# Kernel tuning notes

Measured on AMD Instinct MI355X. Metric: run time of the kernel, lower is better.

Reference implementation:

```python
import jax, jax.numpy as jnp
import numpy as np

A, B, K, P, STRIDE = 32, 32, 3, 4, 2
C = P * P          # 16
D = P * P          # 16 (not last layer)
KK = K * K
KKA = KK * A       # 288
BN_EPS = 1e-5


def _unfold(x, k, s):
    """torch.nn.functional.unfold (pad=0): [b,c,h,w] -> [b, c*k*k, l],
    channel-major then kernel-position ordering (matches torch)."""
    b, c, h, w = x.shape
    oh = (h - k) // s + 1
    ow = (w - k) // s + 1
    patches = jnp.stack(
        [x[:, :, i:i + s * oh:s, j:j + s * ow:s] for i in range(k) for j in range(k)],
        axis=2,
    )  # [b, c, kk, oh, ow]
    return patches.reshape(b, c * k * k, oh * ow)


def setup_inputs() -> dict:
    key = jax.random.key(0)
    k1, k2, k3, k4, k5 = jax.random.split(key, 5)
    b, h, w = 16, 14, 14
    a = jax.random.uniform(k1, (b, A, h, w), dtype=jnp.float32)
    pose = jax.random.normal(k2, (b, A * C, h, w), dtype=jnp.float32)
    # kaiming_uniform over [kkA, B*D, C]: fan_in = C (last dim of matmul weight rows)
    bound1 = float(np.sqrt(6.0 / C))
    W1 = jax.random.uniform(k3, (KKA, B * D, C), minval=-bound1, maxval=bound1, dtype=jnp.float32)
    W2 = jax.random.normal(k4, (KKA, B, C), dtype=jnp.float32) * 0.1
    b2 = jax.random.normal(k5, (1, 1, KKA, B), dtype=jnp.float32) * 0.1
    bn_gamma = jnp.ones((B * D,), dtype=jnp.float32)
    bn_beta = jnp.zeros((B * D,), dtype=jnp.float32)
    return {"a": a, "pose": pose, "W1": W1, "W2": W2, "b2": b2,
            "bn_gamma": bn_gamma, "bn_beta": bn_beta}


def reference(a, pose, W1, W2, b2, bn_gamma, bn_beta):
    b, _, h, w = a.shape
    oh = (h - K) // STRIDE + 1
    ow = (w - K) // STRIDE + 1
    l = oh * ow

    # ---- pose patches: [b, l, kkA, C] (kk-major, A-minor) ----
    pose_u = _unfold(pose, K, STRIDE)                      # [b, A*C*kk, l]
    pose_u = pose_u.reshape(b, A, C, KK, l)
    pose_u = pose_u.transpose(0, 4, 3, 1, 2).reshape(b, l, KKA, C)

    # ---- per-patch small GEMVs ----
    pose_out = jnp.einsum('nmc,blnc->blnm', W1, pose_u)    # [b, l, kkA, B*D]
    pose_out = pose_out.reshape(b, l, KKA, B, D)
    logit = jnp.einsum('njc,blnc->blnj', W2, pose_u) + b2  # [b, l, kkA, B]
    r = jax.nn.softmax(logit, axis=3)

    # ---- activation patches: [b, l, kkA, 1] ----
    a_u = _unfold(a, K, STRIDE).reshape(b, A, KK, l)
    a_u = a_u.transpose(0, 3, 2, 1).reshape(b, l, KKA, 1)

    # ---- routing-weighted reduction ----
    ar = a_u * r                                           # [b, l, kkA, B]
    ar_sum = ar.sum(axis=2, keepdims=True)                 # [b, l, 1, B]
    coeff = (ar / ar_sum)[..., None]                       # [b, l, kkA, B, 1]
    a_out = (ar_sum / a_u.sum(axis=2, keepdims=True)).squeeze(2)  # [b, l, B]
    a_out = a_out.transpose(0, 2, 1).reshape(b, B, oh, ow)

    pose_o = (coeff * pose_out).sum(axis=2)                # [b, l, B, D]
    pose_o = pose_o.reshape(b, l, B * D).transpose(0, 2, 1).reshape(b, B * D, oh, ow)

    # ---- BatchNorm2d (training-mode batch stats, biased var, eps=1e-5) ----
    mean = pose_o.mean(axis=(0, 2, 3), keepdims=True)
    var = pose_o.var(axis=(0, 2, 3), keepdims=True)
    pose_o = (pose_o - mean) * jax.lax.rsqrt(var + BN_EPS)
    pose_o = pose_o * bn_gamma.reshape(1, -1, 1, 1) + bn_beta.reshape(1, -1, 1, 1)
    return a_out, pose_o
```

## Files before the change

### kernel.cpp

```cpp
#include <hip/hip_runtime.h>

#define AA 32
#define BB 32
#define CC 16
#define KKA 288
#define OHW 6
#define LL 36
#define NBL 576
#define HH 14
#define WWD 14

#define W1B_OFF   0ull
#define W2B_OFF   2359296ull
#define PU16_OFF  2506752ull
#define AR16_OFF  5160960ull
#define FREG_BYTE 20938752ull
#define AU_F      0ull
#define ARSUMP_F  165888ull
#define INV_F     497664ull
#define PREP_F    516096ull

typedef __attribute__((ext_vector_type(8))) short bf16x8;
typedef __attribute__((ext_vector_type(4))) float f32x4;
typedef __attribute__((ext_vector_type(16))) float f32x16;

__device__ __forceinline__ unsigned cvtpk(float lo, float hi) {
    unsigned r;
    asm("v_cvt_pk_bf16_f32 %0, %1, %2" : "=v"(r) : "v"(lo), "v"(hi));
    return r;
}
__device__ __forceinline__ float blo(unsigned u) {
    return __builtin_bit_cast(float, u << 16);
}
__device__ __forceinline__ float bhi(unsigned u) {
    return __builtin_bit_cast(float, u & 0xffff0000u);
}

__global__ __launch_bounds__(256) void k_prep(
    const float* __restrict__ W1, const float* __restrict__ W2,
    const float* __restrict__ a, const float* __restrict__ pose,
    unsigned short* __restrict__ W1b, unsigned short* __restrict__ W2b,
    unsigned short* __restrict__ pu16, float* __restrict__ auf)
{
    __shared__ float ps[16][196];
    __shared__ float as_[196];
    const int tid = threadIdx.x;

    if (blockIdx.x < 1224) {
        size_t i = ((size_t)blockIdx.x * 256 + tid) * 8;
        const float* src;
        unsigned short* dst;
        if (i < 2359296ull) { src = W1 + i; dst = W1b + i; }
        else { src = W2 + (i - 2359296ull); dst = W2b + (i - 2359296ull); }
        float4 v0 = *reinterpret_cast<const float4*>(src);
        float4 v1 = *reinterpret_cast<const float4*>(src + 4);
        uint4 o;
        o.x = cvtpk(v0.x, v0.y);
        o.y = cvtpk(v0.z, v0.w);
        o.z = cvtpk(v1.x, v1.y);
        o.w = cvtpk(v1.z, v1.w);
        *reinterpret_cast<uint4*>(dst) = o;
        return;
    }

    const int bid = blockIdx.x - 1224;
    const int b = bid >> 5, aidx = bid & 31;

    const float* psrc = pose + ((size_t)b * 512 + (size_t)aidx * 16) * 196;
    for (int t = tid; t < 3136; t += 256) ((float*)ps)[t] = psrc[t];
    const float* asrc = a + ((size_t)b * 32 + aidx) * 196;
    if (tid < 196) as_[tid] = asrc[tid];
    __syncthreads();

    for (int t = tid; t < 1296; t += 256) {
        int quad = t & 3;
        int l = (t >> 2) % 36;
        int kk = t / 144;
        int oy = l / 6, ox = l - (l / 6) * 6;
        int ki = kk / 3, kj = kk - (kk / 3) * 3;
        int pix = (oy * 2 + ki) * 14 + ox * 2 + kj;
        uint2 v;
        v.x = cvtpk(ps[quad * 4 + 0][pix], ps[quad * 4 + 1][pix]);
        v.y = cvtpk(ps[quad * 4 + 2][pix], ps[quad * 4 + 3][pix]);
        *reinterpret_cast<uint2*>(
            pu16 + (((size_t)(kk * 32 + aidx)) * 576 + b * 36 + l) * 16 + quad * 4) = v;
    }
    for (int t = tid; t < 324; t += 256) {
        int kk = t % 9, l = t / 9;
        int oy = l / 6, ox = l - (l / 6) * 6;
        int ki = kk / 3, kj = kk - (kk / 3) * 3;
        auf[((size_t)(b * 36 + l)) * KKA + kk * 32 + aidx] =
            as_[(oy * 2 + ki) * 14 + ox * 2 + kj];
    }
}

__global__ __launch_bounds__(256) void k_logit(
    const unsigned short* __restrict__ W2b, const unsigned short* __restrict__ pu16,
    const float* __restrict__ b2, const float* __restrict__ auf,
    unsigned* __restrict__ aru, float* __restrict__ arsump)
{
    __shared__ float b2_s[16][32];
    __shared__ float au_s[16][17];
    __shared__ float asum_s[4][16][32];
    const int bl0 = blockIdx.x * 16;
    const int n0b = blockIdx.y * 16;
    const int tid = threadIdx.x;

    #pragma unroll
    for (int k = 0; k < 2; ++k) {
        int t = tid + k * 256;
        b2_s[t >> 5][t & 31] = b2[(size_t)(n0b + (t >> 5)) * 32 + (t & 31)];
    }
    {
        int blr = tid >> 4, nl = tid & 15;
        au_s[blr][nl] = auf[((size_t)(bl0 + blr)) * KKA + n0b + nl];
    }
    __syncthreads();

    const int w = tid >> 6, lane = tid & 63;
    const int g = lane >> 4, d = lane & 15;
    float asum[8] = {0.f, 0.f, 0.f, 0.f, 0.f, 0.f, 0.f, 0.f};

    #pragma unroll
    for (int nn = 0; nn < 4; ++nn) {
        const int nl = w * 4 + nn;
        const int n  = n0b + nl;
        uint4 a0 = {0, 0, 0, 0}, a1 = {0, 0, 0, 0}, bbv = {0, 0, 0, 0};
        if (g < 2) {
            a0 = *reinterpret_cast<const uint4*>(W2b + ((size_t)n * 32 + d) * 16 + g * 8);
            a1 = *reinterpret_cast<const uint4*>(W2b + ((size_t)n * 32 + 16 + d) * 16 + g * 8);
            bbv = *reinterpret_cast<const uint4*>(
                pu16 + ((size_t)n * 576 + bl0 + d) * 16 + g * 8);
        }
        f32x4 zero = {0.f, 0.f, 0.f, 0.f};
        f32x4 c0 = __builtin_amdgcn_mfma_f32_16x16x32_bf16(
            __builtin_bit_cast(bf16x8, a0), __builtin_bit_cast(bf16x8, bbv), zero, 0, 0, 0);
        f32x4 c1 = __builtin_amdgcn_mfma_f32_16x16x32_bf16(
            __builtin_bit_cast(bf16x8, a1), __builtin_bit_cast(bf16x8, bbv), zero, 0, 0, 0);

        float v[8];
        float s = 0.f;
        #pragma unroll
        for (int i = 0; i < 4; ++i) {
            v[i]     = __expf(c0[i] + b2_s[nl][g * 4 + i]);
            v[4 + i] = __expf(c1[i] + b2_s[nl][16 + g * 4 + i]);
            s += v[i] + v[4 + i];
        }
        s += __shfl_xor(s, 16);
        s += __shfl_xor(s, 32);
        const float scale = au_s[d][nl] / s;
        float p[8];
        #pragma unroll
        for (int i = 0; i < 8; ++i) { p[i] = v[i] * scale; asum[i] += p[i]; }

        aru[((size_t)n * 16 + g * 2    ) * 576 + bl0 + d] = cvtpk(p[0], p[1]);
        aru[((size_t)n * 16 + g * 2 + 1) * 576 + bl0 + d] = cvtpk(p[2], p[3]);
        aru[((size_t)n * 16 + 8 + g * 2    ) * 576 + bl0 + d] = cvtpk(p[4], p[5]);
        aru[((size_t)n * 16 + 8 + g * 2 + 1) * 576 + bl0 + d] = cvtpk(p[6], p[7]);
    }
    #pragma unroll
    for (int i = 0; i < 4; ++i) {
        asum_s[w][d][g * 4 + i]      = asum[i];
        asum_s[w][d][16 + g * 4 + i] = asum[4 + i];
    }
    __syncthreads();
    #pragma unroll
    for (int k = 0; k < 2; ++k) {
        int idx = tid + k * 256;
        int dd = idx >> 5, j = idx & 31;
        float s = asum_s[0][dd][j] + asum_s[1][dd][j] + asum_s[2][dd][j] + asum_s[3][dd][j];
        arsump[(size_t)blockIdx.y * 18432 + ((size_t)(bl0 + dd)) * 32 + j] = s;
    }
}

__global__ __launch_bounds__(256) void k_finish(
    const float* __restrict__ arsump, const float* __restrict__ auf,
    float* __restrict__ invarsum, float* __restrict__ out_a)
{
    const int tid = threadIdx.x;
    const int wid = tid >> 6, lane = tid & 63;
    const int bl = blockIdx.x * 4 + wid;
    const int j = lane & 31, h = lane >> 5;

    float s = 0.f;
    #pragma unroll
    for (int k = 0; k < 9; ++k) {
        int r = h * 9 + k;
        s += arsump[(size_t)r * 18432 + (size_t)bl * 32 + j];
    }
    s += __shfl_xor(s, 32);

    float at = 0.f;
    #pragma unroll
    for (int k = 0; k < 5; ++k) {
        int n = k * 64 + lane;
        if (n < KKA) at += auf[(size_t)bl * KKA + n];
    }
    #pragma unroll
    for (int m = 1; m <= 32; m <<= 1) at += __shfl_xor(at, m);

    if (lane < 32) {
        invarsum[(size_t)j * 576 + bl] = 1.0f / s;
        int b = bl / 36, l = bl - (bl / 36) * 36;
        out_a[((size_t)b * 32 + j) * 36 + l] = s / at;
    }
}

__global__ __launch_bounds__(256) void k_pose(
    const unsigned short* __restrict__ W1b, const unsigned short* __restrict__ pu16,
    const unsigned* __restrict__ aru, const float* __restrict__ invarsum,
    float* __restrict__ prep)
{
    __shared__ float red_s[3][16][64];

    const int bid = blockIdx.x;
    const int wg  = (bid & 7) * 144 + (bid >> 3);
    const int q   = wg / 288;
    const int rem = wg - q * 288;
    const int jp  = rem / 18;
    const int bl0 = (rem - jp * 18) * 32;

    const int tid = threadIdx.x;
    const int w = tid >> 6, lane = tid & 63;
    const int col = lane & 31, kg = lane >> 5;

    const unsigned short* wp = W1b + ((size_t)(jp * 32 + col)) * 16 + kg * 8;
    const unsigned short* pp = pu16 + ((size_t)(bl0 + col)) * 16 + kg * 8;
    const unsigned* ap = aru + (size_t)jp * 576 + bl0 + col;
    const int n0 = q * 72 + w * 18;

    float acc[16];
    #pragma unroll
    for (int i = 0; i < 16; ++i) acc[i] = 0.f;
    f32x16 zv = {0.f,0.f,0.f,0.f,0.f,0.f,0.f,0.f,0.f,0.f,0.f,0.f,0.f,0.f,0.f,0.f};

    #pragma unroll 6
    for (int i = 0; i < 18; ++i) {
        const size_t n = (size_t)(n0 + i);
        uint4 a4 = *reinterpret_cast<const uint4*>(wp + n * 8192);
        uint4 b4 = *reinterpret_cast<const uint4*>(pp + n * 9216);
        unsigned av = ap[n * 9216];
        f32x16 cd = __builtin_amdgcn_mfma_f32_32x32x16_bf16(
            __builtin_bit_cast(bf16x8, a4), __builtin_bit_cast(bf16x8, b4),
            zv, 0, 0, 0);
        float slo = blo(av), shi = bhi(av);
        #pragma unroll
        for (int r = 0; r < 8; ++r)  acc[r] = fmaf(cd[r], slo, acc[r]);
        #pragma unroll
        for (int r = 8; r < 16; ++r) acc[r] = fmaf(cd[r], shi, acc[r]);
    }

    if (w > 0) {
        #pragma unroll
        for (int i = 0; i < 16; ++i) red_s[w - 1][i][lane] = acc[i];
    }
    __syncthreads();
    if (w == 0) {
        const float ilo = invarsum[(size_t)(jp * 2) * 576 + bl0 + col];
        const float ihi = invarsum[(size_t)(jp * 2 + 1) * 576 + bl0 + col];
        #pragma unroll
        for (int i = 0; i < 16; ++i) {
            float v = acc[i] + red_s[0][i][lane] + red_s[1][i][lane] + red_s[2][i][lane];
            int r = (i & 3) + 8 * (i >> 2) + 4 * kg;
            float vv = v * (i < 8 ? ilo : ihi);
            prep[((size_t)q * 512 + jp * 32 + r) * NBL + bl0 + col] = vv;
        }
    }
}

__global__ __launch_bounds__(256) void k_bn(
    const float* __restrict__ prep, const float* __restrict__ gamma,
    const float* __restrict__ beta, float* __restrict__ out_pose)
{
    const int tid = threadIdx.x;
    const int wid = tid >> 6, lane = tid & 63;
    const int ch  = blockIdx.x * 4 + wid;
    const float* p0 = prep + (size_t)ch * NBL;

    float sum = 0.f, sq = 0.f;
    float v[9];
    #pragma unroll
    for (int k = 0; k < 9; ++k) {
        int i = lane + k * 64;
        float x = p0[i] + p0[i + 294912] + p0[i + 2 * 294912] + p0[i + 3 * 294912];
        v[k] = x;
        sum += x;
        sq  += x * x;
    }
    #pragma unroll
    for (int msk = 32; msk >= 1; msk >>= 1) {
        sum += __shfl_xor(sum, msk);
        sq  += __shfl_xor(sq, msk);
    }
    const float mean = sum * (1.f / 576.f);
    const float var  = sq * (1.f / 576.f) - mean * mean;
    const float inv  = rsqrtf(var + 1e-5f);
    const float sc   = gamma[ch] * inv;
    const float sh   = beta[ch] - mean * sc;
    #pragma unroll
    for (int k = 0; k < 9; ++k) {
        int i = lane + k * 64;
        int b = i / 36;
        int l = i - b * 36;
        out_pose[(size_t)b * 18432 + (size_t)ch * 36 + l] = v[k] * sc + sh;
    }
}

extern "C" void kernel_launch(void* const* d_in, const int* in_sizes, int n_in,
                              void* d_out, int out_size, void* d_ws, size_t ws_size,
                              hipStream_t stream)
{
    const float* a     = (const float*)d_in[0];
    const float* pose  = (const float*)d_in[1];
    const float* W1    = (const float*)d_in[2];
    const float* W2    = (const float*)d_in[3];
    const float* b2    = (const float*)d_in[4];
    const float* gamma = (const float*)d_in[5];
    const float* beta  = (const float*)d_in[6];
    float* out      = (float*)d_out;
    float* out_a    = out;
    float* out_pose = out + 18432;

    unsigned short* wsu = (unsigned short*)d_ws;
    unsigned short* W1b   = wsu + W1B_OFF;
    unsigned short* W2b   = wsu + W2B_OFF;
    unsigned short* pu16  = wsu + PU16_OFF;
    unsigned*       aru   = (unsigned*)(wsu + AR16_OFF);
    float* wsf    = (float*)((char*)d_ws + FREG_BYTE);
    float* auf    = wsf + AU_F;
    float* arsump = wsf + ARSUMP_F;
    float* invv   = wsf + INV_F;
    float* prep   = wsf + PREP_F;

    hipLaunchKernelGGL(k_prep, dim3(1736), dim3(256), 0, stream,
                       W1, W2, a, pose, W1b, W2b, pu16, auf);
    hipLaunchKernelGGL(k_logit, dim3(36, 18), dim3(256), 0, stream,
                       W2b, pu16, b2, auf, aru, arsump);
    hipLaunchKernelGGL(k_finish, dim3(144), dim3(256), 0, stream,
                       arsump, auf, invv, out_a);
    hipLaunchKernelGGL(k_pose, dim3(1152), dim3(256), 0, stream,
                       W1b, pu16, aru, invv, prep);
    hipLaunchKernelGGL(k_bn, dim3(128), dim3(256), 0, stream,
                       prep, gamma, beta, out_pose);
}
```

Baseline: 38.99 us.

## Remove k_finish kernel by folding arsum reduction into k_pose and k_bn

The logit kernel moves from 16x16x32 MFMA tiles to a single 32x32x16 MFMA per n and writes its partial ar sums in a j-major [r][j][bl] layout. The separate k_finish launch is removed. k_pose now reduces the 36 partial sums itself to form the inverse ar_sum, and k_bn gains 16 extra blocks that compute a_out. This saves one kernel launch and its dependency barrier, but repeats the partial-sum reduction in every k_pose workgroup.

```diff
diff --git a/kernel.cpp b/kernel.cpp
--- a/kernel.cpp
+++ b/kernel.cpp
@@ -17,8 +17,7 @@
 #define FREG_BYTE 20938752ull
 #define AU_F      0ull
 #define ARSUMP_F  165888ull
-#define INV_F     497664ull
-#define PREP_F    516096ull
+#define PREP_F    829440ull
 
 typedef __attribute__((ext_vector_type(8))) short bf16x8;
 typedef __attribute__((ext_vector_type(4))) float f32x4;
@@ -99,116 +98,82 @@
     const float* __restrict__ b2, const float* __restrict__ auf,
     unsigned* __restrict__ aru, float* __restrict__ arsump)
 {
-    __shared__ float b2_s[16][32];
-    __shared__ float au_s[16][17];
-    __shared__ float asum_s[4][16][32];
-    const int bl0 = blockIdx.x * 16;
-    const int n0b = blockIdx.y * 16;
+    __shared__ float b2_s[8][32];
+    __shared__ float au_s[8][32];
+    __shared__ float asum_s[4][64][16];
+
+    const int bl0 = blockIdx.x * 32;
+    const int n0  = blockIdx.y * 8;
     const int tid = threadIdx.x;
-
-    #pragma unroll
-    for (int k = 0; k < 2; ++k) {
-        int t = tid + k * 256;
-        b2_s[t >> 5][t & 31] = b2[(size_t)(n0b + (t >> 5)) * 32 + (t & 31)];
-    }
+    const int w = tid >> 6, lane = tid & 63;
+    const int col = lane & 31, kg = lane >> 5;
+
     {
-        int blr = tid >> 4, nl = tid & 15;
-        au_s[blr][nl] = auf[((size_t)(bl0 + blr)) * KKA + n0b + nl];
-    }
-    __syncthreads();
-
-    const int w = tid >> 6, lane = tid & 63;
-    const int g = lane >> 4, d = lane & 15;
-    float asum[8] = {0.f, 0.f, 0.f, 0.f, 0.f, 0.f, 0.f, 0.f};
-
-    #pragma unroll
-    for (int nn = 0; nn < 4; ++nn) {
-        const int nl = w * 4 + nn;
-        const int n  = n0b + nl;
-        uint4 a0 = {0, 0, 0, 0}, a1 = {0, 0, 0, 0}, bbv = {0, 0, 0, 0};
-        if (g < 2) {
-            a0 = *reinterpret_cast<const uint4*>(W2b + ((size_t)n * 32 + d) * 16 + g * 8);
-            a1 = *reinterpret_cast<const uint4*>(W2b + ((size_t)n * 32 + 16 + d) * 16 + g * 8);
-            bbv = *reinterpret_cast<const uint4*>(
-                pu16 + ((size_t)n * 576 + bl0 + d) * 16 + g * 8);
-        }
-        f32x4 zero = {0.f, 0.f, 0.f, 0.f};
-        f32x4 c0 = __builtin_amdgcn_mfma_f32_16x16x32_bf16(
-            __builtin_bit_cast(bf16x8, a0), __builtin_bit_cast(bf16x8, bbv), zero, 0, 0, 0);
-        f32x4 c1 = __builtin_amdgcn_mfma_f32_16x16x32_bf16(
-            __builtin_bit_cast(bf16x8, a1), __builtin_bit_cast(bf16x8, bbv), zero, 0, 0, 0);
-
-        float v[8];
+        int nl = tid >> 5, j = tid & 31;
+        b2_s[nl][j] = b2[(size_t)(n0 + nl) * 32 + j];
+        int nl2 = tid & 7, blr = tid >> 3;
+        au_s[nl2][blr] = auf[((size_t)(bl0 + blr)) * KKA + n0 + nl2];
+    }
+    __syncthreads();
+
+    float asum[16];
+    #pragma unroll
+    for (int i = 0; i < 16; ++i) asum[i] = 0.f;
+    const f32x16 zv = {0.f,0.f,0.f,0.f,0.f,0.f,0.f,0.f,
+                       0.f,0.f,0.f,0.f,0.f,0.f,0.f,0.f};
+
+    #pragma unroll
+    for (int nn = 0; nn < 2; ++nn) {
+        const int nl = w * 2 + nn;
+        const int n  = n0 + nl;
+        uint4 a4 = *reinterpret_cast<const uint4*>(
+            W2b + ((size_t)n * 32 + col) * 16 + kg * 8);
+        uint4 b4 = *reinterpret_cast<const uint4*>(
+            pu16 + ((size_t)n * 576 + bl0 + col) * 16 + kg * 8);
+        f32x16 cd = __builtin_amdgcn_mfma_f32_32x32x16_bf16(
+            __builtin_bit_cast(bf16x8, a4), __builtin_bit_cast(bf16x8, b4),
+            zv, 0, 0, 0);
+
+        float p[16];
         float s = 0.f;
         #pragma unroll
-        for (int i = 0; i < 4; ++i) {
-            v[i]     = __expf(c0[i] + b2_s[nl][g * 4 + i]);
-            v[4 + i] = __expf(c1[i] + b2_s[nl][16 + g * 4 + i]);
-            s += v[i] + v[4 + i];
-        }
-        s += __shfl_xor(s, 16);
+        for (int m = 0; m < 4; ++m) {
+            float4 bb = *reinterpret_cast<const float4*>(&b2_s[nl][m * 8 + kg * 4]);
+            p[m * 4 + 0] = __expf(cd[m * 4 + 0] + bb.x);
+            p[m * 4 + 1] = __expf(cd[m * 4 + 1] + bb.y);
+            p[m * 4 + 2] = __expf(cd[m * 4 + 2] + bb.z);
+            p[m * 4 + 3] = __expf(cd[m * 4 + 3] + bb.w);
+            s += p[m*4+0] + p[m*4+1] + p[m*4+2] + p[m*4+3];
+        }
         s += __shfl_xor(s, 32);
-        const float scale = au_s[d][nl] / s;
-        float p[8];
-        #pragma unroll
-        for (int i = 0; i < 8; ++i) { p[i] = v[i] * scale; asum[i] += p[i]; }
-
-        aru[((size_t)n * 16 + g * 2    ) * 576 + bl0 + d] = cvtpk(p[0], p[1]);
-        aru[((size_t)n * 16 + g * 2 + 1) * 576 + bl0 + d] = cvtpk(p[2], p[3]);
-        aru[((size_t)n * 16 + 8 + g * 2    ) * 576 + bl0 + d] = cvtpk(p[4], p[5]);
-        aru[((size_t)n * 16 + 8 + g * 2 + 1) * 576 + bl0 + d] = cvtpk(p[6], p[7]);
-    }
-    #pragma unroll
-    for (int i = 0; i < 4; ++i) {
-        asum_s[w][d][g * 4 + i]      = asum[i];
-        asum_s[w][d][16 + g * 4 + i] = asum[4 + i];
-    }
-    __syncthreads();
-    #pragma unroll
-    for (int k = 0; k < 2; ++k) {
+        const float scale = au_s[nl][col] / s;
+        #pragma unroll
+        for (int i = 0; i < 16; ++i) { p[i] *= scale; asum[i] += p[i]; }
+
+        #pragma unroll
+        for (int t = 0; t < 8; ++t) {
+            int jp = (t & 1) + 4 * (t >> 1) + 2 * kg;
+            aru[((size_t)n * 16 + jp) * 576 + bl0 + col] =
+                cvtpk(p[2 * t], p[2 * t + 1]);
+        }
+    }
+    #pragma unroll
+    for (int i = 0; i < 16; ++i) asum_s[w][lane][i] = asum[i];
+    __syncthreads();
+    #pragma unroll
+    for (int k = 0; k < 4; ++k) {
         int idx = tid + k * 256;
-        int dd = idx >> 5, j = idx & 31;
-        float s = asum_s[0][dd][j] + asum_s[1][dd][j] + asum_s[2][dd][j] + asum_s[3][dd][j];
-        arsump[(size_t)blockIdx.y * 18432 + ((size_t)(bl0 + dd)) * 32 + j] = s;
-    }
-}
-
-__global__ __launch_bounds__(256) void k_finish(
-    const float* __restrict__ arsump, const float* __restrict__ auf,
-    float* __restrict__ invarsum, float* __restrict__ out_a)
-{
-    const int tid = threadIdx.x;
-    const int wid = tid >> 6, lane = tid & 63;
-    const int bl = blockIdx.x * 4 + wid;
-    const int j = lane & 31, h = lane >> 5;
-
-    float s = 0.f;
-    #pragma unroll
-    for (int k = 0; k < 9; ++k) {
-        int r = h * 9 + k;
-        s += arsump[(size_t)r * 18432 + (size_t)bl * 32 + j];
-    }
-    s += __shfl_xor(s, 32);
-
-    float at = 0.f;
-    #pragma unroll
-    for (int k = 0; k < 5; ++k) {
-        int n = k * 64 + lane;
-        if (n < KKA) at += auf[(size_t)bl * KKA + n];
-    }
-    #pragma unroll
-    for (int m = 1; m <= 32; m <<= 1) at += __shfl_xor(at, m);
-
-    if (lane < 32) {
-        invarsum[(size_t)j * 576 + bl] = 1.0f / s;
-        int b = bl / 36, l = bl - (bl / 36) * 36;
-        out_a[((size_t)b * 32 + j) * 36 + l] = s / at;
+        int L = idx & 63, i = idx >> 6;
+        float s = asum_s[0][L][i] + asum_s[1][L][i]
+                + asum_s[2][L][i] + asum_s[3][L][i];
+        int row = (i & 3) + 8 * (i >> 2) + 4 * (L >> 5);
+        arsump[((size_t)blockIdx.y * 32 + row) * 576 + bl0 + (L & 31)] = s;
     }
 }
 
 __global__ __launch_bounds__(256) void k_pose(
     const unsigned short* __restrict__ W1b, const unsigned short* __restrict__ pu16,
-    const unsigned* __restrict__ aru, const float* __restrict__ invarsum,
+    const unsigned* __restrict__ aru, const float* __restrict__ arsump,
     float* __restrict__ prep)
 {
     __shared__ float red_s[3][16][64];
@@ -223,6 +188,17 @@
     const int tid = threadIdx.x;
     const int w = tid >> 6, lane = tid & 63;
     const int col = lane & 31, kg = lane >> 5;
+
+    float ilo = 0.f, ihi = 0.f;
+    if (w == 0) {
+        #pragma unroll 9
+        for (int r = 0; r < 36; ++r) {
+            ilo += arsump[((size_t)r * 32 + jp * 2    ) * 576 + bl0 + col];
+            ihi += arsump[((size_t)r * 32 + jp * 2 + 1) * 576 + bl0 + col];
+        }
+        ilo = 1.0f / ilo;
+        ihi = 1.0f / ihi;
+    }
 
     const unsigned short* wp = W1b + ((size_t)(jp * 32 + col)) * 16 + kg * 8;
     const unsigned short* pp = pu16 + ((size_t)(bl0 + col)) * 16 + kg * 8;
@@ -256,8 +232,6 @@
     }
     __syncthreads();
     if (w == 0) {
-        const float ilo = invarsum[(size_t)(jp * 2) * 576 + bl0 + col];
-        const float ihi = invarsum[(size_t)(jp * 2 + 1) * 576 + bl0 + col];
         #pragma unroll
         for (int i = 0; i < 16; ++i) {
             float v = acc[i] + red_s[0][i][lane] + red_s[1][i][lane] + red_s[2][i][lane];
@@ -270,39 +244,66 @@
 
 __global__ __launch_bounds__(256) void k_bn(
     const float* __restrict__ prep, const float* __restrict__ gamma,
-    const float* __restrict__ beta, float* __restrict__ out_pose)
-{
+    const float* __restrict__ beta, const float* __restrict__ arsump,
+    const float* __restrict__ auf, float* __restrict__ out_pose,
+    float* __restrict__ out_a)
+{
+    __shared__ float atot_s[36];
     const int tid = threadIdx.x;
     const int wid = tid >> 6, lane = tid & 63;
-    const int ch  = blockIdx.x * 4 + wid;
-    const float* p0 = prep + (size_t)ch * NBL;
-
-    float sum = 0.f, sq = 0.f;
-    float v[9];
-    #pragma unroll
-    for (int k = 0; k < 9; ++k) {
-        int i = lane + k * 64;
-        float x = p0[i] + p0[i + 294912] + p0[i + 2 * 294912] + p0[i + 3 * 294912];
-        v[k] = x;
-        sum += x;
-        sq  += x * x;
-    }
-    #pragma unroll
-    for (int msk = 32; msk >= 1; msk >>= 1) {
-        sum += __shfl_xor(sum, msk);
-        sq  += __shfl_xor(sq, msk);
-    }
-    const float mean = sum * (1.f / 576.f);
-    const float var  = sq * (1.f / 576.f) - mean * mean;
-    const float inv  = rsqrtf(var + 1e-5f);
-    const float sc   = gamma[ch] * inv;
-    const float sh   = beta[ch] - mean * sc;
-    #pragma unroll
-    for (int k = 0; k < 9; ++k) {
-        int i = lane + k * 64;
-        int b = i / 36;
-        int l = i - b * 36;
-        out_pose[(size_t)b * 18432 + (size_t)ch * 36 + l] = v[k] * sc + sh;
+
+    if (blockIdx.x < 128) {
+        const int ch = blockIdx.x * 4 + wid;
+        const float* p0 = prep + (size_t)ch * NBL;
+
+        float sum = 0.f, sq = 0.f;
+        float v[9];
+        #pragma unroll
+        for (int k = 0; k < 9; ++k) {
+            int i = lane + k * 64;
+            float x = p0[i] + p0[i + 294912] + p0[i + 2 * 294912] + p0[i + 3 * 294912];
+            v[k] = x;
+            sum += x;
+            sq  += x * x;
+        }
+        #pragma unroll
+        for (int msk = 32; msk >= 1; msk >>= 1) {
+            sum += __shfl_xor(sum, msk);
+            sq  += __shfl_xor(sq, msk);
+        }
+        const float mean = sum * (1.f / 576.f);
+        const float var  = sq * (1.f / 576.f) - mean * mean;
+        const float inv  = rsqrtf(var + 1e-5f);
+        const float sc   = gamma[ch] * inv;
+        const float sh   = beta[ch] - mean * sc;
+        #pragma unroll
+        for (int k = 0; k < 9; ++k) {
+            int i = lane + k * 64;
+            int b = i / 36;
+            int l = i - b * 36;
+            out_pose[(size_t)b * 18432 + (size_t)ch * 36 + l] = v[k] * sc + sh;
+        }
+        return;
+    }
+
+    const int b = blockIdx.x - 128;
+    for (int l = wid; l < 36; l += 4) {
+        const int bl = b * 36 + l;
+        float p = 0.f;
+        for (int k = lane; k < KKA; k += 64) p += auf[(size_t)bl * KKA + k];
+        #pragma unroll
+        for (int m = 1; m <= 32; m <<= 1) p += __shfl_xor(p, m);
+        if (lane == 0) atot_s[l] = p;
+    }
+    __syncthreads();
+    for (int t = tid; t < 1152; t += 256) {
+        int l = t >> 5, j = t & 31;
+        int bl = b * 36 + l;
+        float s = 0.f;
+        #pragma unroll 9
+        for (int r = 0; r < 36; ++r)
+            s += arsump[((size_t)r * 32 + j) * 576 + bl];
+        out_a[((size_t)b * 32 + j) * 36 + l] = s / atot_s[l];
     }
 }
 
@@ -329,17 +330,14 @@
     float* wsf    = (float*)((char*)d_ws + FREG_BYTE);
     float* auf    = wsf + AU_F;
     float* arsump = wsf + ARSUMP_F;
-    float* invv   = wsf + INV_F;
     float* prep   = wsf + PREP_F;
 
     hipLaunchKernelGGL(k_prep, dim3(1736), dim3(256), 0, stream,
                        W1, W2, a, pose, W1b, W2b, pu16, auf);
-    hipLaunchKernelGGL(k_logit, dim3(36, 18), dim3(256), 0, stream,
+    hipLaunchKernelGGL(k_logit, dim3(18, 36), dim3(256), 0, stream,
                        W2b, pu16, b2, auf, aru, arsump);
-    hipLaunchKernelGGL(k_finish, dim3(144), dim3(256), 0, stream,
-                       arsump, auf, invv, out_a);
     hipLaunchKernelGGL(k_pose, dim3(1152), dim3(256), 0, stream,
-                       W1b, pu16, aru, invv, prep);
-    hipLaunchKernelGGL(k_bn, dim3(128), dim3(256), 0, stream,
-                       prep, gamma, beta, out_pose);
-}
+                       W1b, pu16, aru, arsump, prep);
+    hipLaunchKernelGGL(k_bn, dim3(144), dim3(256), 0, stream,
+                       prep, gamma, beta, arsump, auf, out_pose, out_a);
+}
```

Measured after the change: 71.67 us. 83.8% more time.
